# Kernel tuning notes

Measured on AMD Instinct MI355X. Metric: run time of the kernel, lower is better.

## Reference

```python
import jax, jax.numpy as jnp
import numpy as np

N, E, H = 50000, 800000, 4
IN, HID, OUT = 128, 64, 16
SIM_THRESH = 0.1
NEG_SLOPE = 0.01  # F.leaky_relu default


def setup_inputs() -> dict:
    key = jax.random.key(0)
    k = jax.random.split(key, 6)
    x = jax.random.normal(k[0], (N, IN), jnp.float32)
    row = jax.random.randint(k[1], (E,), 0, N)
    col = jax.random.randint(k[2], (E,), 0, N)
    W0 = jax.random.normal(k[3], (H, IN, HID), jnp.float32) / np.float32(np.sqrt(IN))
    W1 = jax.random.normal(k[4], (H, H * HID, HID), jnp.float32) / np.float32(np.sqrt(H * HID))
    W2 = jax.random.normal(k[5], (1, H * HID, OUT), jnp.float32) / np.float32(np.sqrt(H * HID))
    return {"x": x, "W0": W0, "W1": W1, "W2": W2, "row": row, "col": col}


def _att_coef(x, row, col):
    # cosine similarity on edges only (honors the sparse edge structure)
    nrm = jnp.linalg.norm(x, axis=1, keepdims=True)
    xn = x / jnp.maximum(nrm, 1e-12)
    sim = jnp.sum(xn[row] * xn[col], axis=1)            # [E]
    sim = jnp.where(sim < SIM_THRESH, 0.0, sim)
    # L1 row-normalize the thresholded attention matrix
    rowsum = jax.ops.segment_sum(jnp.abs(sim), row, num_segments=N)
    rs_e = rowsum[row]
    att = jnp.where(rs_e > 0, sim / jnp.where(rs_e > 0, rs_e, 1.0), 0.0)
    # degree-based self-loop weight lam = 1/(deg+1), then exp of all nonzeros
    deg = jax.ops.segment_sum((att != 0).astype(x.dtype), row, num_segments=N)
    w_edge = jnp.where(att != 0, jnp.exp(att), 0.0)     # zero entries stay zero (dropped nnz)
    w_self = jnp.exp(1.0 / (deg + 1.0))                 # [N]
    return w_edge, w_self


def _layer(x, W, row, col, act):
    w_edge, w_self = _att_coef(x, row, col)
    z = jnp.einsum('nd,hdo->nho', x, W)                 # per-head projection
    msg = w_edge[:, None, None] * z[col]                # [E,h,o] gather + weight
    agg = jax.ops.segment_sum(msg, row, num_segments=N) + w_self[:, None, None] * z
    out = agg.reshape(N, -1)                            # concat heads (flatten(1))
    return jax.nn.leaky_relu(out, NEG_SLOPE) if act else out


def reference(x, W0, W1, W2, row, col):
    h = _layer(x, W0, row, col, True)
    h = _layer(h, W1, row, col, True)
    h = _layer(h, W2, row, col, False)
    return h
```

## Files before the change

### kernel.cpp

```cpp
#include <hip/hip_runtime.h>
#include <math.h>


static inline int cdiv(int a, int b){ return (a + b - 1) / b; }


__device__ inline float vdot(float4 a, float4 b){ return a.x*b.x + a.y*b.y + a.z*b.z + a.w*b.w; }
__device__ inline void vfma(float4& acc, float w, float4 b){
  acc.x += w*b.x; acc.y += w*b.y; acc.z += w*b.z; acc.w += w*b.w;
}
__device__ inline float4 vscale(float w, float4 a){ return make_float4(w*a.x, w*a.y, w*a.z, w*a.w); }

__device__ inline float wred(float d){
  #pragma unroll
  for (int off = 32; off; off >>= 1) d += __shfl_xor(d, off);
  return d;
}

__device__ inline unsigned short f2bf(float f){
  unsigned int u = __float_as_uint(f);
  unsigned int r = (u + 0x7FFFu + ((u >> 16) & 1u)) >> 16;
  return (unsigned short)r;
}
__device__ inline float bf2f(unsigned int us){ return __uint_as_float(us << 16); }

__device__ inline void bf8_to_f(uint4 v, float* f){
  f[0] = bf2f(v.x & 0xFFFFu); f[1] = bf2f(v.x >> 16);
  f[2] = bf2f(v.y & 0xFFFFu); f[3] = bf2f(v.y >> 16);
  f[4] = bf2f(v.z & 0xFFFFu); f[5] = bf2f(v.z >> 16);
  f[6] = bf2f(v.w & 0xFFFFu); f[7] = bf2f(v.w >> 16);
}


__global__ void count_kernel(const int* __restrict__ row, int* __restrict__ cnt, int E){
  int e = blockIdx.x * blockDim.x + threadIdx.x;
  if (e < E) atomicAdd(&cnt[row[e]], 1);
}

__global__ void scan1_kernel(const int* __restrict__ cnt, int* __restrict__ offs,
                             int* __restrict__ bsum, int n){
  __shared__ int tmp[256];
  int tid = threadIdx.x;
  int g = blockIdx.x * 256 + tid;
  int v = (g < n) ? cnt[g] : 0;
  tmp[tid] = v;
  __syncthreads();
  for (int off = 1; off < 256; off <<= 1){
    int t = (tid >= off) ? tmp[tid - off] : 0;
    __syncthreads();
    tmp[tid] += t;
    __syncthreads();
  }
  if (g < n) offs[g] = tmp[tid] - v;
  if (tid == 255) bsum[blockIdx.x] = tmp[255];
}

__global__ void scan2_kernel(int* __restrict__ bsum, int* __restrict__ offs, int nb, int n){
  __shared__ int tmp[256];
  int tid = threadIdx.x;
  int v = (tid < nb) ? bsum[tid] : 0;
  tmp[tid] = v;
  __syncthreads();
  for (int off = 1; off < 256; off <<= 1){
    int t = (tid >= off) ? tmp[tid - off] : 0;
    __syncthreads();
    tmp[tid] += t;
    __syncthreads();
  }
  if (tid < nb) bsum[tid] = tmp[tid] - v;
  if (tid == 255) offs[n] = tmp[255];
}

__global__ void scan3_kernel(int* __restrict__ offs, int* __restrict__ cur,
                             const int* __restrict__ bsum, int n){
  int g = blockIdx.x * 256 + threadIdx.x;
  if (g < n){
    int o = offs[g] + bsum[blockIdx.x];
    offs[g] = o;
    cur[g]  = o;
  }
}

__global__ void scatter_kernel(const int* __restrict__ row, const int* __restrict__ col,
                               int* __restrict__ cur, int* __restrict__ ecol, int E){
  int e = blockIdx.x * blockDim.x + threadIdx.x;
  if (e < E){
    int p = atomicAdd(&cur[row[e]], 1);
    ecol[p] = col[e];
  }
}


__global__ void invnorm128_kernel(const float* __restrict__ x, float* __restrict__ invn, int N){
  int n = blockIdx.x * 4 + (threadIdx.x >> 6);
  int lane = threadIdx.x & 63;
  if (n >= N) return;
  float2 a = ((const float2*)(x + (size_t)n * 128))[lane];
  float ss = a.x * a.x + a.y * a.y;
  ss = wred(ss);
  if (lane == 0) invn[n] = 1.0f / fmaxf(sqrtf(ss), 1e-12f);
}


template<int R>
__global__ void att_agg_wave128(const float* __restrict__ x, const float* __restrict__ invn,
                                const int* __restrict__ offs, const int* __restrict__ ecol,
                                float* __restrict__ out, int N){
  constexpr int LT = 64;
  __shared__ float tls[4][LT];
  __shared__ int   tlk[4][LT];
  const int wid  = threadIdx.x >> 6;
  const int lane = threadIdx.x & 63;
  const int half = lane >> 5, hl = lane & 31;
  const int hidx = wid * 2 + half;
  const int n = blockIdx.x * 2 + wid;
  if (n >= N) return;
  const int s = offs[n], e = offs[n + 1];
  const float inr = invn[n];
  const float4* xv = (const float4*)x;
  float4 a = xv[(size_t)n * 32 + hl];

  float4 br[R];
  float  simv[R];
  float  rowsum = 0.0f;
  int    deg = 0;

  #pragma unroll
  for (int r = 0; r < R; r++){
    simv[r] = 0.0f;
    int k = s + 2 * r + half;
    if (k < e){
      int c = ecol[k];
      float4 b = xv[(size_t)c * 32 + hl];
      br[r] = b;
      float d = vdot(a, b);
      #pragma unroll
      for (int off = 16; off; off >>= 1) d += __shfl_xor(d, off);
      d *= inr * invn[c];
      if (d < 0.1f) d = 0.0f;
      simv[r] = d;
      rowsum += d;
      deg += (d != 0.0f) ? 1 : 0;
    }
  }

  int tc = 0, kover = e;
  int k = s + 2 * R + half;
  for (; k + 2 < e; k += 4){
    int c0 = ecol[k], c1 = ecol[k + 2];
    float4 b0 = xv[(size_t)c0 * 32 + hl];
    float4 b1 = xv[(size_t)c1 * 32 + hl];
    float d0 = vdot(a, b0), d1 = vdot(a, b1);
    #pragma unroll
    for (int off = 16; off; off >>= 1){ d0 += __shfl_xor(d0, off); d1 += __shfl_xor(d1, off); }
    d0 *= inr * invn[c0];
    d1 *= inr * invn[c1];
    if (d0 < 0.1f) d0 = 0.0f;
    if (d1 < 0.1f) d1 = 0.0f;
    rowsum += d0 + d1;
    deg += (d0 != 0.0f) + (d1 != 0.0f);
    if (d0 > 0.0f){
      if (tc < LT){ if (hl == 0){ tls[hidx][tc] = d0; tlk[hidx][tc] = c0; } tc++; }
      else if (kover > k) kover = k;
    }
    if (d1 > 0.0f){
      if (tc < LT){ if (hl == 0){ tls[hidx][tc] = d1; tlk[hidx][tc] = c1; } tc++; }
      else if (kover > k + 2) kover = k + 2;
    }
  }
  if (k < e){
    int c0 = ecol[k];
    float4 b0 = xv[(size_t)c0 * 32 + hl];
    float d0 = vdot(a, b0);
    #pragma unroll
    for (int off = 16; off; off >>= 1) d0 += __shfl_xor(d0, off);
    d0 *= inr * invn[c0];
    if (d0 < 0.1f) d0 = 0.0f;
    rowsum += d0;
    deg += (d0 != 0.0f) ? 1 : 0;
    if (d0 > 0.0f){
      if (tc < LT){ if (hl == 0){ tls[hidx][tc] = d0; tlk[hidx][tc] = c0; } tc++; }
      else if (kover > k) kover = k;
    }
  }

  rowsum += __shfl_xor(rowsum, 32);
  deg    += __shfl_xor(deg, 32);
  const float invrs = (rowsum > 0.0f) ? 1.0f / rowsum : 0.0f;
  const float wself = expf(1.0f / (float)(deg + 1));

  float4 acc = (half == 0) ? vscale(wself, a) : make_float4(0.f, 0.f, 0.f, 0.f);
  #pragma unroll
  for (int r = 0; r < R; r++){
    if (simv[r] > 0.0f) vfma(acc, expf(simv[r] * invrs), br[r]);
  }
  int j = 0;
  for (; j + 1 < tc; j += 2){
    float w0 = expf(tls[hidx][j] * invrs);
    float w1 = expf(tls[hidx][j + 1] * invrs);
    int c0 = tlk[hidx][j], c1 = tlk[hidx][j + 1];
    float4 b0 = xv[(size_t)c0 * 32 + hl];
    float4 b1 = xv[(size_t)c1 * 32 + hl];
    vfma(acc, w0, b0);
    vfma(acc, w1, b1);
  }
  if (j < tc){
    float w0 = expf(tls[hidx][j] * invrs);
    float4 b0 = xv[(size_t)tlk[hidx][j] * 32 + hl];
    vfma(acc, w0, b0);
  }
  for (int k2 = kover; k2 < e; k2 += 2){
    int c = ecol[k2];
    float4 b = xv[(size_t)c * 32 + hl];
    float d = vdot(a, b);
    #pragma unroll
    for (int off = 16; off; off >>= 1) d += __shfl_xor(d, off);
    d *= inr * invn[c];
    if (d >= 0.1f) vfma(acc, expf(d * invrs), b);
  }

  acc.x += __shfl_xor(acc.x, 32);
  acc.y += __shfl_xor(acc.y, 32);
  acc.z += __shfl_xor(acc.z, 32);
  acc.w += __shfl_xor(acc.w, 32);
  if (half == 0) ((float4*)out)[(size_t)n * 32 + hl] = acc;
}


template<int R>
__global__ void att256_bf(const unsigned short* __restrict__ hbf,
                          const float* __restrict__ invn,
                          const int* __restrict__ offs, const int* __restrict__ ecol,
                          float* __restrict__ out, int N){
  constexpr int LT = 64;
  __shared__ float tls[4][LT];
  __shared__ int   tlk[4][LT];
  const int wid  = threadIdx.x >> 6;
  const int lane = threadIdx.x & 63;
  const int half = lane >> 5, hl = lane & 31;
  const int hidx = wid * 2 + half;
  const int n = blockIdx.x * 2 + wid;
  if (n >= N) return;
  const int s = offs[n], e = offs[n + 1];
  const float inr = invn[n];
  const uint4* hb = (const uint4*)hbf;

  float a8[8];
  bf8_to_f(hb[(size_t)n * 32 + hl], a8);

  uint4 brv[R];
  float simv[R];
  float rowsum = 0.0f;
  int   deg = 0;

  #pragma unroll
  for (int r = 0; r < R; r++){
    simv[r] = 0.0f;
    int k = s + 2 * r + half;
    if (k < e){
      int c = ecol[k];
      uint4 v = hb[(size_t)c * 32 + hl];
      brv[r] = v;
      float b8[8]; bf8_to_f(v, b8);
      float d = 0.0f;
      #pragma unroll
      for (int t = 0; t < 8; t++) d += a8[t] * b8[t];
      #pragma unroll
      for (int off = 16; off; off >>= 1) d += __shfl_xor(d, off);
      d *= inr * invn[c];
      if (d < 0.1f) d = 0.0f;
      simv[r] = d;
      rowsum += d;
      deg += (d != 0.0f) ? 1 : 0;
    }
  }

  int tc = 0, kover = e;
  int k = s + 2 * R + half;
  for (; k + 2 < e; k += 4){
    int c0 = ecol[k], c1 = ecol[k + 2];
    uint4 v0 = hb[(size_t)c0 * 32 + hl];
    uint4 v1 = hb[(size_t)c1 * 32 + hl];
    float b0[8], b1[8];
    bf8_to_f(v0, b0);
    bf8_to_f(v1, b1);
    float d0 = 0.0f, d1 = 0.0f;
    #pragma unroll
    for (int t = 0; t < 8; t++){ d0 += a8[t] * b0[t]; d1 += a8[t] * b1[t]; }
    #pragma unroll
    for (int off = 16; off; off >>= 1){ d0 += __shfl_xor(d0, off); d1 += __shfl_xor(d1, off); }
    d0 *= inr * invn[c0];
    d1 *= inr * invn[c1];
    if (d0 < 0.1f) d0 = 0.0f;
    if (d1 < 0.1f) d1 = 0.0f;
    rowsum += d0 + d1;
    deg += (d0 != 0.0f) + (d1 != 0.0f);
    if (d0 > 0.0f){
      if (tc < LT){ if (hl == 0){ tls[hidx][tc] = d0; tlk[hidx][tc] = c0; } tc++; }
      else if (kover > k) kover = k;
    }
    if (d1 > 0.0f){
      if (tc < LT){ if (hl == 0){ tls[hidx][tc] = d1; tlk[hidx][tc] = c1; } tc++; }
      else if (kover > k + 2) kover = k + 2;
    }
  }
  if (k < e){
    int c0 = ecol[k];
    uint4 v0 = hb[(size_t)c0 * 32 + hl];
    float b0[8]; bf8_to_f(v0, b0);
    float d0 = 0.0f;
    #pragma unroll
    for (int t = 0; t < 8; t++) d0 += a8[t] * b0[t];
    #pragma unroll
    for (int off = 16; off; off >>= 1) d0 += __shfl_xor(d0, off);
    d0 *= inr * invn[c0];
    if (d0 < 0.1f) d0 = 0.0f;
    rowsum += d0;
    deg += (d0 != 0.0f) ? 1 : 0;
    if (d0 > 0.0f){
      if (tc < LT){ if (hl == 0){ tls[hidx][tc] = d0; tlk[hidx][tc] = c0; } tc++; }
      else if (kover > k) kover = k;
    }
  }

  rowsum += __shfl_xor(rowsum, 32);
  deg    += __shfl_xor(deg, 32);
  const float invrs = (rowsum > 0.0f) ? 1.0f / rowsum : 0.0f;
  const float wself = expf(1.0f / (float)(deg + 1));

  float acc8[8];
  #pragma unroll
  for (int t = 0; t < 8; t++) acc8[t] = (half == 0) ? wself * a8[t] : 0.0f;
  #pragma unroll
  for (int r = 0; r < R; r++){
    if (simv[r] > 0.0f){
      float w = expf(simv[r] * invrs);
      float b8[8]; bf8_to_f(brv[r], b8);
      #pragma unroll
      for (int t = 0; t < 8; t++) acc8[t] += w * b8[t];
    }
  }
  int j = 0;
  for (; j + 1 < tc; j += 2){
    float w0 = expf(tls[hidx][j] * invrs);
    float w1 = expf(tls[hidx][j + 1] * invrs);
    uint4 v0 = hb[(size_t)tlk[hidx][j] * 32 + hl];
    uint4 v1 = hb[(size_t)tlk[hidx][j + 1] * 32 + hl];
    float b0[8], b1[8];
    bf8_to_f(v0, b0);
    bf8_to_f(v1, b1);
    #pragma unroll
    for (int t = 0; t < 8; t++) acc8[t] += w0 * b0[t] + w1 * b1[t];
  }
  if (j < tc){
    float w0 = expf(tls[hidx][j] * invrs);
    uint4 v0 = hb[(size_t)tlk[hidx][j] * 32 + hl];
    float b0[8]; bf8_to_f(v0, b0);
    #pragma unroll
    for (int t = 0; t < 8; t++) acc8[t] += w0 * b0[t];
  }
  for (int k2 = kover; k2 < e; k2 += 2){
    int c = ecol[k2];
    uint4 v = hb[(size_t)c * 32 + hl];
    float b[8]; bf8_to_f(v, b);
    float d = 0.0f;
    #pragma unroll
    for (int t = 0; t < 8; t++) d += a8[t] * b[t];
    #pragma unroll
    for (int off = 16; off; off >>= 1) d += __shfl_xor(d, off);
    d *= inr * invn[c];
    if (d >= 0.1f){
      float w = expf(d * invrs);
      #pragma unroll
      for (int t = 0; t < 8; t++) acc8[t] += w * b[t];
    }
  }

  #pragma unroll
  for (int t = 0; t < 8; t++) acc8[t] += __shfl_xor(acc8[t], 32);
  if (half == 0){
    float4* ov = (float4*)out;
    ov[(size_t)n * 64 + 2 * hl]     = make_float4(acc8[0], acc8[1], acc8[2], acc8[3]);
    ov[(size_t)n * 64 + 2 * hl + 1] = make_float4(acc8[4], acc8[5], acc8[6], acc8[7]);
  }
}


__global__ void att_z16_bf(const unsigned short* __restrict__ hbf,
                           const float* __restrict__ invn,
                           const int* __restrict__ offs, const int* __restrict__ ecol,
                           const float* __restrict__ z2, float* __restrict__ out, int N){
  constexpr int LT = 64;
  __shared__ float tls[4][LT];
  __shared__ int   tlk[4][LT];
  const int wid  = threadIdx.x >> 6;
  const int lane = threadIdx.x & 63;
  const int half = lane >> 5, hl = lane & 31;
  const int hidx = wid * 2 + half;
  const int n = blockIdx.x * 2 + wid;
  if (n >= N) return;
  const int s = offs[n], e = offs[n + 1];
  const float inr = invn[n];
  const uint4* hb = (const uint4*)hbf;

  float a8[8];
  bf8_to_f(hb[(size_t)n * 32 + hl], a8);

  float rowsum = 0.0f;
  int   deg = 0;
  int   tc = 0, kover = e;

  int k = s + half;
  for (; k + 2 < e; k += 4){
    int c0 = ecol[k], c1 = ecol[k + 2];
    uint4 v0 = hb[(size_t)c0 * 32 + hl];
    uint4 v1 = hb[(size_t)c1 * 32 + hl];
    float b0[8], b1[8];
    bf8_to_f(v0, b0);
    bf8_to_f(v1, b1);
    float d0 = 0.0f, d1 = 0.0f;
    #pragma unroll
    for (int t = 0; t < 8; t++){ d0 += a8[t] * b0[t]; d1 += a8[t] * b1[t]; }
    #pragma unroll
    for (int off = 16; off; off >>= 1){ d0 += __shfl_xor(d0, off); d1 += __shfl_xor(d1, off); }
    d0 *= inr * invn[c0];
    d1 *= inr * invn[c1];
    if (d0 < 0.1f) d0 = 0.0f;
    if (d1 < 0.1f) d1 = 0.0f;
    rowsum += d0 + d1;
    deg += (d0 != 0.0f) + (d1 != 0.0f);
    if (d0 > 0.0f){
      if (tc < LT){ if (hl == 0){ tls[hidx][tc] = d0; tlk[hidx][tc] = c0; } tc++; }
      else if (kover > k) kover = k;
    }
    if (d1 > 0.0f){
      if (tc < LT){ if (hl == 0){ tls[hidx][tc] = d1; tlk[hidx][tc] = c1; } tc++; }
      else if (kover > k + 2) kover = k + 2;
    }
  }
  if (k < e){
    int c0 = ecol[k];
    uint4 v0 = hb[(size_t)c0 * 32 + hl];
    float b0[8]; bf8_to_f(v0, b0);
    float d0 = 0.0f;
    #pragma unroll
    for (int t = 0; t < 8; t++) d0 += a8[t] * b0[t];
    #pragma unroll
    for (int off = 16; off; off >>= 1) d0 += __shfl_xor(d0, off);
    d0 *= inr * invn[c0];
    if (d0 < 0.1f) d0 = 0.0f;
    rowsum += d0;
    deg += (d0 != 0.0f) ? 1 : 0;
    if (d0 > 0.0f){
      if (tc < LT){ if (hl == 0){ tls[hidx][tc] = d0; tlk[hidx][tc] = c0; } tc++; }
      else if (kover > k) kover = k;
    }
  }

  rowsum += __shfl_xor(rowsum, 32);
  deg    += __shfl_xor(deg, 32);
  const float invrs = (rowsum > 0.0f) ? 1.0f / rowsum : 0.0f;
  const float wself = expf(1.0f / (float)(deg + 1));

  const int grp = hl >> 4, ch = hl & 15;
  float acc = 0.0f;
  for (int j = grp; j < tc; j += 2){
    float w = expf(tls[hidx][j] * invrs);
    int   c = tlk[hidx][j];
    acc += w * z2[(size_t)c * 16 + ch];
  }
  for (int k2 = kover; k2 < e; k2 += 2){
    int c = ecol[k2];
    uint4 v = hb[(size_t)c * 32 + hl];
    float b[8]; bf8_to_f(v, b);
    float d = 0.0f;
    #pragma unroll
    for (int t = 0; t < 8; t++) d += a8[t] * b[t];
    #pragma unroll
    for (int off = 16; off; off >>= 1) d += __shfl_xor(d, off);
    d *= inr * invn[c];
    if (d >= 0.1f){
      float w = expf(d * invrs);
      if (grp == 0) acc += w * z2[(size_t)c * 16 + ch];
    }
  }
  acc += __shfl_xor(acc, 16);
  acc += __shfl_xor(acc, 32);
  if (lane < 16) out[(size_t)n * 16 + lane] = acc + wself * z2[(size_t)n * 16 + lane];
}


template<int D>
__global__ __launch_bounds__(256) void proj_act_norm(
    const float* __restrict__ xin, const float* __restrict__ W,
    float* __restrict__ hout, float* __restrict__ invn,
    unsigned short* __restrict__ hbf, int N){
  __shared__ float xs[32][D];
  const int tid = threadIdx.x;
  const int w = tid >> 6, l = tid & 63;
  const int n0 = blockIdx.x * 32;

  {
    float4* xs4 = (float4*)&xs[0][0];
    const float4* xin4 = (const float4*)(xin + (size_t)n0 * D);
    const int rows = (N - n0 >= 32) ? 32 : (N - n0);
    const int limit4 = rows * (D / 4);
    constexpr int total4 = 32 * D / 4;
    for (int i = tid; i < total4; i += 256)
      xs4[i] = (i < limit4) ? xin4[i] : make_float4(0.f, 0.f, 0.f, 0.f);
  }
  __syncthreads();

  const int h  = l >> 4;
  const int oo = (l & 15) * 4;
  const float* Wp = W + (size_t)h * D * 64 + oo;
  const float* xrow = &xs[w * 8][0];

  float acc[8][4];
  #pragma unroll
  for (int i = 0; i < 8; i++){
    acc[i][0] = 0.f; acc[i][1] = 0.f; acc[i][2] = 0.f; acc[i][3] = 0.f;
  }

  for (int d = 0; d < D; d += 4){
    float4 w0 = *(const float4*)(Wp + (size_t)(d + 0) * 64);
    float4 w1 = *(const float4*)(Wp + (size_t)(d + 1) * 64);
    float4 w2 = *(const float4*)(Wp + (size_t)(d + 2) * 64);
    float4 w3 = *(const float4*)(Wp + (size_t)(d + 3) * 64);
    #pragma unroll
    for (int i = 0; i < 8; i++){
      float4 xv = *(const float4*)(xrow + i * D + d);
      acc[i][0] += xv.x * w0.x + xv.y * w1.x + xv.z * w2.x + xv.w * w3.x;
      acc[i][1] += xv.x * w0.y + xv.y * w1.y + xv.z * w2.y + xv.w * w3.y;
      acc[i][2] += xv.x * w0.z + xv.y * w1.z + xv.z * w2.z + xv.w * w3.z;
      acc[i][3] += xv.x * w0.w + xv.y * w1.w + xv.z * w2.w + xv.w * w3.w;
    }
  }

  const int nrow = n0 + w * 8;
  #pragma unroll
  for (int i = 0; i < 8; i++){
    #pragma unroll
    for (int j = 0; j < 4; j++){
      float a = acc[i][j];
      acc[i][j] = (a > 0.0f) ? a : 0.01f * a;
    }
    float ss = acc[i][0]*acc[i][0] + acc[i][1]*acc[i][1]
             + acc[i][2]*acc[i][2] + acc[i][3]*acc[i][3];
    ss = wred(ss);
    const int n = nrow + i;
    if (n < N){
      if (l == 0) invn[n] = 1.0f / fmaxf(sqrtf(ss), 1e-12f);
      ((float4*)hout)[(size_t)n * 64 + l] =
          make_float4(acc[i][0], acc[i][1], acc[i][2], acc[i][3]);
      if (hbf){
        ushort4 u;
        u.x = f2bf(acc[i][0]); u.y = f2bf(acc[i][1]);
        u.z = f2bf(acc[i][2]); u.w = f2bf(acc[i][3]);
        ((ushort4*)hbf)[(size_t)n * 64 + l] = u;
      }
    }
  }
}

__global__ void proj16_kernel(const float* __restrict__ x, const float* __restrict__ W,
                              float* __restrict__ z, int N){
  __shared__ float xs[16][256];
  __shared__ float wsh[256 * 16];
  int tid = threadIdx.x;
  int n0 = blockIdx.x * 16;
  for (int i = tid; i < 16 * 256; i += 256){
    int nl = i >> 8, d = i & 255;
    int n = n0 + nl;
    xs[nl][d] = (n < N) ? x[(size_t)n * 256 + d] : 0.0f;
  }
  for (int i = tid; i < 256 * 16; i += 256) wsh[i] = W[i];
  __syncthreads();
  int nl = tid >> 4, o = tid & 15;
  float acc = 0.0f;
  for (int d = 0; d < 256; d++) acc += xs[nl][d] * wsh[d * 16 + o];
  int n = n0 + nl;
  if (n < N) z[(size_t)n * 16 + o] = acc;
}


extern "C" void kernel_launch(void* const* d_in, const int* in_sizes, int n_in,
                              void* d_out, int out_size, void* d_ws, size_t ws_size,
                              hipStream_t stream){
  const float* x  = (const float*)d_in[0];
  const float* W0 = (const float*)d_in[1];
  const float* W1 = (const float*)d_in[2];
  const float* W2 = (const float*)d_in[3];
  const int*   row = (const int*)d_in[4];
  const int*   col = (const int*)d_in[5];
  const int N = in_sizes[0] / 128;
  const int E = in_sizes[4];
  float* out = (float*)d_out;

  float* p = (float*)d_ws;
  float* hbuf   = p; p += (size_t)N * 256;
  float* aggbuf = p; p += (size_t)N * 256;
  float* z2     = p; p += (size_t)N * 16;
  float* invn   = p; p += N;
  unsigned short* hbf = (unsigned short*)p; p += (size_t)N * 128;
  int* cnt  = (int*)p;
  int* offs = cnt + N;
  int* cur  = offs + N + 1;
  int* ecol = cur + N;
  int* bsum = ecol + E;

  const int NB = cdiv(N, 256);

  hipMemsetAsync(cnt, 0, sizeof(int) * N, stream);
  count_kernel<<<cdiv(E, 256), 256, 0, stream>>>(row, cnt, E);
  scan1_kernel<<<NB, 256, 0, stream>>>(cnt, offs, bsum, N);
  scan2_kernel<<<1, 256, 0, stream>>>(bsum, offs, NB, N);
  scan3_kernel<<<NB, 256, 0, stream>>>(offs, cur, bsum, N);
  scatter_kernel<<<cdiv(E, 256), 256, 0, stream>>>(row, col, cur, ecol, E);

  invnorm128_kernel<<<cdiv(N, 4), 256, 0, stream>>>(x, invn, N);
  att_agg_wave128<8><<<cdiv(N, 2), 128, 0, stream>>>(x, invn, offs, ecol, aggbuf, N);
  proj_act_norm<128><<<cdiv(N, 32), 256, 0, stream>>>(aggbuf, W0, hbuf, invn, hbf, N);

  att256_bf<4><<<cdiv(N, 2), 128, 0, stream>>>(hbf, invn, offs, ecol, aggbuf, N);
  proj_act_norm<256><<<cdiv(N, 32), 256, 0, stream>>>(aggbuf, W1, hbuf, invn, hbf, N);

  proj16_kernel<<<cdiv(N, 16), 256, 0, stream>>>(hbuf, W2, z2, N);
  att_z16_bf<<<cdiv(N, 2), 128, 0, stream>>>(hbf, invn, offs, ecol, z2, out, N);
}
```

Before: 667.8 us.

## Compute edge cosine similarities with bf16 MFMA in layer-2 and layer-3 attention

```diff
diff --git a/kernel.cpp b/kernel.cpp
--- a/kernel.cpp
+++ b/kernel.cpp
@@ -30,6 +30,9 @@
   f[4] = bf2f(v.z & 0xFFFFu); f[5] = bf2f(v.z >> 16);
   f[6] = bf2f(v.w & 0xFFFFu); f[7] = bf2f(v.w >> 16);
 }
+
+typedef __attribute__((ext_vector_type(8))) short bf16x8;
+typedef __attribute__((ext_vector_type(4))) float f32x4;
 
 
 __global__ void count_kernel(const int* __restrict__ row, int* __restrict__ cnt, int E){
@@ -227,141 +230,128 @@
 }
 
 
-template<int R>
-__global__ void att256_bf(const unsigned short* __restrict__ hbf,
-                          const float* __restrict__ invn,
-                          const int* __restrict__ offs, const int* __restrict__ ecol,
-                          float* __restrict__ out, int N){
-  constexpr int LT = 64;
-  __shared__ float tls[4][LT];
-  __shared__ int   tlk[4][LT];
-  const int wid  = threadIdx.x >> 6;
-  const int lane = threadIdx.x & 63;
-  const int half = lane >> 5, hl = lane & 31;
-  const int hidx = wid * 2 + half;
+template<int LT>
+__device__ inline void sim_rows_mfma(const uint4* __restrict__ hb4,
+                                     const float* __restrict__ invn,
+                                     const int* __restrict__ ecol,
+                                     int n, int s, int e, float inr,
+                                     float* __restrict__ tls, int* __restrict__ tlk,
+                                     float& rowsum_o, int& deg_o, int& tcl_o, int& kover_o){
+  const int l = threadIdx.x & 63;
+  const int g = l >> 4;
+  const bf16x8* hbv = (const bf16x8*)hb4;
+
+  bf16x8 bfrag[8];
+  #pragma unroll
+  for (int f = 0; f < 8; f++) bfrag[f] = hbv[(size_t)n * 32 + f * 4 + g];
+
+  float rowsum = 0.0f;
+  int deg = 0, tc = 0, kover = e;
+
+  for (int k0 = s; k0 < e; k0 += 16){
+    int idx = k0 + (l & 15);
+    int kk = (idx < e) ? idx : (e - 1);
+    int c_l = ecol[kk];
+    float ic_l = invn[c_l];
+    const size_t cb = (size_t)c_l * 32 + g;
+    f32x4 acc0 = {0.f, 0.f, 0.f, 0.f};
+    f32x4 acc1 = {0.f, 0.f, 0.f, 0.f};
+    #pragma unroll
+    for (int f = 0; f < 8; f += 2){
+      bf16x8 av0 = hbv[cb + (size_t)f * 4];
+      bf16x8 av1 = hbv[cb + (size_t)(f + 1) * 4];
+      acc0 = __builtin_amdgcn_mfma_f32_16x16x32_bf16(av0, bfrag[f],     acc0, 0, 0, 0);
+      acc1 = __builtin_amdgcn_mfma_f32_16x16x32_bf16(av1, bfrag[f + 1], acc1, 0, 0, 0);
+    }
+    float dv[4]; int cm[4];
+    int bits = 0;
+    #pragma unroll
+    for (int r = 0; r < 4; r++){
+      int m = g * 4 + r;
+      cm[r] = __shfl(c_l, m);
+      float ic = __shfl(ic_l, m);
+      float d = (acc0[r] + acc1[r]) * inr * ic;
+      if (d < 0.1f || (k0 + m) >= e) d = 0.0f;
+      dv[r] = d;
+      rowsum += d;
+      deg += (d != 0.0f) ? 1 : 0;
+      if (d > 0.0f) bits |= (1 << r);
+    }
+    int M16 = bits << (g * 4);
+    M16 |= __shfl_xor(M16, 16);
+    M16 |= __shfl_xor(M16, 32);
+    #pragma unroll
+    for (int r = 0; r < 4; r++){
+      if ((l & 15) == 0 && dv[r] > 0.0f){
+        int m = g * 4 + r;
+        int pos = tc + __popc(M16 & ((1 << m) - 1));
+        if (pos < LT){ tls[pos] = dv[r]; tlk[pos] = cm[r]; }
+        else if (k0 + m < kover) kover = k0 + m;
+      }
+    }
+    tc += __popc(M16);
+  }
+  rowsum += __shfl_xor(rowsum, 16);
+  rowsum += __shfl_xor(rowsum, 32);
+  deg    += __shfl_xor(deg, 16);
+  deg    += __shfl_xor(deg, 32);
+  #pragma unroll
+  for (int off = 32; off; off >>= 1) kover = min(kover, __shfl_xor(kover, off));
+  rowsum_o = rowsum; deg_o = deg;
+  tcl_o = (tc < LT) ? tc : LT;
+  kover_o = kover;
+}
+
+
+template<int LT>
+__global__ __launch_bounds__(128) void att256_mfma(
+    const unsigned short* __restrict__ hbf, const float* __restrict__ invn,
+    const int* __restrict__ offs, const int* __restrict__ ecol,
+    float* __restrict__ out, int N){
+  __shared__ float tls[2][LT];
+  __shared__ int   tlk[2][LT];
+  const int wid = threadIdx.x >> 6;
+  const int l   = threadIdx.x & 63;
   const int n = blockIdx.x * 2 + wid;
   if (n >= N) return;
   const int s = offs[n], e = offs[n + 1];
   const float inr = invn[n];
-  const uint4* hb = (const uint4*)hbf;
-
-  float a8[8];
-  bf8_to_f(hb[(size_t)n * 32 + hl], a8);
-
-  uint4 brv[R];
-  float simv[R];
-  float rowsum = 0.0f;
-  int   deg = 0;
-
-  #pragma unroll
-  for (int r = 0; r < R; r++){
-    simv[r] = 0.0f;
-    int k = s + 2 * r + half;
-    if (k < e){
-      int c = ecol[k];
-      uint4 v = hb[(size_t)c * 32 + hl];
-      brv[r] = v;
-      float b8[8]; bf8_to_f(v, b8);
-      float d = 0.0f;
-      #pragma unroll
-      for (int t = 0; t < 8; t++) d += a8[t] * b8[t];
-      #pragma unroll
-      for (int off = 16; off; off >>= 1) d += __shfl_xor(d, off);
-      d *= inr * invn[c];
-      if (d < 0.1f) d = 0.0f;
-      simv[r] = d;
-      rowsum += d;
-      deg += (d != 0.0f) ? 1 : 0;
-    }
-  }
-
-  int tc = 0, kover = e;
-  int k = s + 2 * R + half;
-  for (; k + 2 < e; k += 4){
-    int c0 = ecol[k], c1 = ecol[k + 2];
-    uint4 v0 = hb[(size_t)c0 * 32 + hl];
-    uint4 v1 = hb[(size_t)c1 * 32 + hl];
-    float b0[8], b1[8];
-    bf8_to_f(v0, b0);
-    bf8_to_f(v1, b1);
-    float d0 = 0.0f, d1 = 0.0f;
-    #pragma unroll
-    for (int t = 0; t < 8; t++){ d0 += a8[t] * b0[t]; d1 += a8[t] * b1[t]; }
-    #pragma unroll
-    for (int off = 16; off; off >>= 1){ d0 += __shfl_xor(d0, off); d1 += __shfl_xor(d1, off); }
-    d0 *= inr * invn[c0];
-    d1 *= inr * invn[c1];
-    if (d0 < 0.1f) d0 = 0.0f;
-    if (d1 < 0.1f) d1 = 0.0f;
-    rowsum += d0 + d1;
-    deg += (d0 != 0.0f) + (d1 != 0.0f);
-    if (d0 > 0.0f){
-      if (tc < LT){ if (hl == 0){ tls[hidx][tc] = d0; tlk[hidx][tc] = c0; } tc++; }
-      else if (kover > k) kover = k;
-    }
-    if (d1 > 0.0f){
-      if (tc < LT){ if (hl == 0){ tls[hidx][tc] = d1; tlk[hidx][tc] = c1; } tc++; }
-      else if (kover > k + 2) kover = k + 2;
-    }
-  }
-  if (k < e){
-    int c0 = ecol[k];
-    uint4 v0 = hb[(size_t)c0 * 32 + hl];
-    float b0[8]; bf8_to_f(v0, b0);
-    float d0 = 0.0f;
-    #pragma unroll
-    for (int t = 0; t < 8; t++) d0 += a8[t] * b0[t];
-    #pragma unroll
-    for (int off = 16; off; off >>= 1) d0 += __shfl_xor(d0, off);
-    d0 *= inr * invn[c0];
-    if (d0 < 0.1f) d0 = 0.0f;
-    rowsum += d0;
-    deg += (d0 != 0.0f) ? 1 : 0;
-    if (d0 > 0.0f){
-      if (tc < LT){ if (hl == 0){ tls[hidx][tc] = d0; tlk[hidx][tc] = c0; } tc++; }
-      else if (kover > k) kover = k;
-    }
-  }
-
-  rowsum += __shfl_xor(rowsum, 32);
-  deg    += __shfl_xor(deg, 32);
+  const uint4* hb4 = (const uint4*)hbf;
+
+  float rowsum; int deg, tcl, kover;
+  sim_rows_mfma<LT>(hb4, invn, ecol, n, s, e, inr, tls[wid], tlk[wid],
+                    rowsum, deg, tcl, kover);
+
   const float invrs = (rowsum > 0.0f) ? 1.0f / rowsum : 0.0f;
   const float wself = expf(1.0f / (float)(deg + 1));
 
+  const int half = l >> 5, hl = l & 31;
+  float a8[8]; bf8_to_f(hb4[(size_t)n * 32 + hl], a8);
   float acc8[8];
   #pragma unroll
   for (int t = 0; t < 8; t++) acc8[t] = (half == 0) ? wself * a8[t] : 0.0f;
-  #pragma unroll
-  for (int r = 0; r < R; r++){
-    if (simv[r] > 0.0f){
-      float w = expf(simv[r] * invrs);
-      float b8[8]; bf8_to_f(brv[r], b8);
-      #pragma unroll
-      for (int t = 0; t < 8; t++) acc8[t] += w * b8[t];
-    }
-  }
-  int j = 0;
-  for (; j + 1 < tc; j += 2){
-    float w0 = expf(tls[hidx][j] * invrs);
-    float w1 = expf(tls[hidx][j + 1] * invrs);
-    uint4 v0 = hb[(size_t)tlk[hidx][j] * 32 + hl];
-    uint4 v1 = hb[(size_t)tlk[hidx][j + 1] * 32 + hl];
+
+  int j = half;
+  for (; j + 2 < tcl; j += 4){
+    float w0 = expf(tls[wid][j] * invrs);
+    float w1 = expf(tls[wid][j + 2] * invrs);
+    uint4 v0 = hb4[(size_t)tlk[wid][j] * 32 + hl];
+    uint4 v1 = hb4[(size_t)tlk[wid][j + 2] * 32 + hl];
     float b0[8], b1[8];
-    bf8_to_f(v0, b0);
-    bf8_to_f(v1, b1);
+    bf8_to_f(v0, b0); bf8_to_f(v1, b1);
     #pragma unroll
     for (int t = 0; t < 8; t++) acc8[t] += w0 * b0[t] + w1 * b1[t];
   }
-  if (j < tc){
-    float w0 = expf(tls[hidx][j] * invrs);
-    uint4 v0 = hb[(size_t)tlk[hidx][j] * 32 + hl];
+  if (j < tcl){
+    float w0 = expf(tls[wid][j] * invrs);
+    uint4 v0 = hb4[(size_t)tlk[wid][j] * 32 + hl];
     float b0[8]; bf8_to_f(v0, b0);
     #pragma unroll
     for (int t = 0; t < 8; t++) acc8[t] += w0 * b0[t];
   }
-  for (int k2 = kover; k2 < e; k2 += 2){
+  for (int k2 = kover; k2 < e; k2++){
     int c = ecol[k2];
-    uint4 v = hb[(size_t)c * 32 + hl];
+    uint4 v = hb4[(size_t)c * 32 + hl];
     float b[8]; bf8_to_f(v, b);
     float d = 0.0f;
     #pragma unroll
@@ -369,7 +359,7 @@
     #pragma unroll
     for (int off = 16; off; off >>= 1) d += __shfl_xor(d, off);
     d *= inr * invn[c];
-    if (d >= 0.1f){
+    if (d >= 0.1f && half == 0){
       float w = expf(d * invrs);
       #pragma unroll
       for (int t = 0; t < 8; t++) acc8[t] += w * b[t];
@@ -386,107 +376,54 @@
 }
 
 
-__global__ void att_z16_bf(const unsigned short* __restrict__ hbf,
-                           const float* __restrict__ invn,
-                           const int* __restrict__ offs, const int* __restrict__ ecol,
-                           const float* __restrict__ z2, float* __restrict__ out, int N){
-  constexpr int LT = 64;
-  __shared__ float tls[4][LT];
-  __shared__ int   tlk[4][LT];
-  const int wid  = threadIdx.x >> 6;
-  const int lane = threadIdx.x & 63;
-  const int half = lane >> 5, hl = lane & 31;
-  const int hidx = wid * 2 + half;
+template<int LT>
+__global__ __launch_bounds__(128) void attz16_mfma(
+    const unsigned short* __restrict__ hbf, const float* __restrict__ invn,
+    const int* __restrict__ offs, const int* __restrict__ ecol,
+    const float* __restrict__ z2, float* __restrict__ out, int N){
+  __shared__ float tls[2][LT];
+  __shared__ int   tlk[2][LT];
+  const int wid = threadIdx.x >> 6;
+  const int l   = threadIdx.x & 63;
   const int n = blockIdx.x * 2 + wid;
   if (n >= N) return;
   const int s = offs[n], e = offs[n + 1];
   const float inr = invn[n];
-  const uint4* hb = (const uint4*)hbf;
-
-  float a8[8];
-  bf8_to_f(hb[(size_t)n * 32 + hl], a8);
-
-  float rowsum = 0.0f;
-  int   deg = 0;
-  int   tc = 0, kover = e;
-
-  int k = s + half;
-  for (; k + 2 < e; k += 4){
-    int c0 = ecol[k], c1 = ecol[k + 2];
-    uint4 v0 = hb[(size_t)c0 * 32 + hl];
-    uint4 v1 = hb[(size_t)c1 * 32 + hl];
-    float b0[8], b1[8];
-    bf8_to_f(v0, b0);
-    bf8_to_f(v1, b1);
-    float d0 = 0.0f, d1 = 0.0f;
-    #pragma unroll
-    for (int t = 0; t < 8; t++){ d0 += a8[t] * b0[t]; d1 += a8[t] * b1[t]; }
-    #pragma unroll
-    for (int off = 16; off; off >>= 1){ d0 += __shfl_xor(d0, off); d1 += __shfl_xor(d1, off); }
-    d0 *= inr * invn[c0];
-    d1 *= inr * invn[c1];
-    if (d0 < 0.1f) d0 = 0.0f;
-    if (d1 < 0.1f) d1 = 0.0f;
-    rowsum += d0 + d1;
-    deg += (d0 != 0.0f) + (d1 != 0.0f);
-    if (d0 > 0.0f){
-      if (tc < LT){ if (hl == 0){ tls[hidx][tc] = d0; tlk[hidx][tc] = c0; } tc++; }
-      else if (kover > k) kover = k;
-    }
-    if (d1 > 0.0f){
-      if (tc < LT){ if (hl == 0){ tls[hidx][tc] = d1; tlk[hidx][tc] = c1; } tc++; }
-      else if (kover > k + 2) kover = k + 2;
-    }
-  }
-  if (k < e){
-    int c0 = ecol[k];
-    uint4 v0 = hb[(size_t)c0 * 32 + hl];
-    float b0[8]; bf8_to_f(v0, b0);
-    float d0 = 0.0f;
-    #pragma unroll
-    for (int t = 0; t < 8; t++) d0 += a8[t] * b0[t];
-    #pragma unroll
-    for (int off = 16; off; off >>= 1) d0 += __shfl_xor(d0, off);
-    d0 *= inr * invn[c0];
-    if (d0 < 0.1f) d0 = 0.0f;
-    rowsum += d0;
-    deg += (d0 != 0.0f) ? 1 : 0;
-    if (d0 > 0.0f){
-      if (tc < LT){ if (hl == 0){ tls[hidx][tc] = d0; tlk[hidx][tc] = c0; } tc++; }
-      else if (kover > k) kover = k;
-    }
-  }
-
-  rowsum += __shfl_xor(rowsum, 32);
-  deg    += __shfl_xor(deg, 32);
+  const uint4* hb4 = (const uint4*)hbf;
+
+  float rowsum; int deg, tcl, kover;
+  sim_rows_mfma<LT>(hb4, invn, ecol, n, s, e, inr, tls[wid], tlk[wid],
+                    rowsum, deg, tcl, kover);
+
   const float invrs = (rowsum > 0.0f) ? 1.0f / rowsum : 0.0f;
   const float wself = expf(1.0f / (float)(deg + 1));
 
-  const int grp = hl >> 4, ch = hl & 15;
+  const int g = l >> 4, ch = l & 15;
   float acc = 0.0f;
-  for (int j = grp; j < tc; j += 2){
-    float w = expf(tls[hidx][j] * invrs);
-    int   c = tlk[hidx][j];
-    acc += w * z2[(size_t)c * 16 + ch];
-  }
-  for (int k2 = kover; k2 < e; k2 += 2){
-    int c = ecol[k2];
-    uint4 v = hb[(size_t)c * 32 + hl];
-    float b[8]; bf8_to_f(v, b);
-    float d = 0.0f;
-    #pragma unroll
-    for (int t = 0; t < 8; t++) d += a8[t] * b[t];
-    #pragma unroll
-    for (int off = 16; off; off >>= 1) d += __shfl_xor(d, off);
-    d *= inr * invn[c];
-    if (d >= 0.1f){
-      float w = expf(d * invrs);
-      if (grp == 0) acc += w * z2[(size_t)c * 16 + ch];
+  for (int j = g; j < tcl; j += 4){
+    float w = expf(tls[wid][j] * invrs);
+    acc += w * z2[(size_t)tlk[wid][j] * 16 + ch];
+  }
+  if (kover < e){
+    const int hl = l & 31;
+    float a8[8]; bf8_to_f(hb4[(size_t)n * 32 + hl], a8);
+    for (int k2 = kover; k2 < e; k2++){
+      int c = ecol[k2];
+      uint4 v = hb4[(size_t)c * 32 + hl];
+      float b[8]; bf8_to_f(v, b);
+      float d = 0.0f;
+      #pragma unroll
+      for (int t = 0; t < 8; t++) d += a8[t] * b[t];
+      #pragma unroll
+      for (int off = 16; off; off >>= 1) d += __shfl_xor(d, off);
+      d *= inr * invn[c];
+      if (d >= 0.1f && g == 0)
+        acc += expf(d * invrs) * z2[(size_t)c * 16 + ch];
     }
   }
   acc += __shfl_xor(acc, 16);
   acc += __shfl_xor(acc, 32);
-  if (lane < 16) out[(size_t)n * 16 + lane] = acc + wself * z2[(size_t)n * 16 + lane];
+  if (l < 16) out[(size_t)n * 16 + l] = acc + wself * z2[(size_t)n * 16 + l];
 }
 
 
@@ -622,9 +559,9 @@
   att_agg_wave128<8><<<cdiv(N, 2), 128, 0, stream>>>(x, invn, offs, ecol, aggbuf, N);
   proj_act_norm<128><<<cdiv(N, 32), 256, 0, stream>>>(aggbuf, W0, hbuf, invn, hbf, N);
 
-  att256_bf<4><<<cdiv(N, 2), 128, 0, stream>>>(hbf, invn, offs, ecol, aggbuf, N);
+  att256_mfma<256><<<cdiv(N, 2), 128, 0, stream>>>(hbf, invn, offs, ecol, aggbuf, N);
   proj_act_norm<256><<<cdiv(N, 32), 256, 0, stream>>>(aggbuf, W1, hbuf, invn, hbf, N);
 
   proj16_kernel<<<cdiv(N, 16), 256, 0, stream>>>(hbuf, W2, z2, N);
-  att_z16_bf<<<cdiv(N, 2), 128, 0, stream>>>(hbf, invn, offs, ecol, z2, out, N);
-}
+  attz16_mfma<256><<<cdiv(N, 2), 128, 0, stream>>>(hbf, invn, offs, ecol, z2, out, N);
+}
```

After: 690.9 us. 3.5% more time.
